# Optimization experiments

Measured on AMD Instinct MI355X. Metric: run time of the kernel, lower is better.

The kernel has to match this reference:

```python
import jax, jax.numpy as jnp
import numpy as np


def _knn(coords, k):
    # coords: [N, 3]. Returns indices of the k nearest neighbors (self excluded): [N, k]
    sq = jnp.sum(coords * coords, axis=1)
    d2 = sq[:, None] + sq[None, :] - 2.0 * (coords @ coords.T)  # [N, N]
    n = coords.shape[0]
    d2 = jnp.where(jnp.eye(n, dtype=bool), jnp.inf, d2)  # loop=False: no self edges
    _, idx = jax.lax.top_k(-d2, k)
    return idx


def setup_inputs() -> dict:
    key = jax.random.key(0)
    ks = jax.random.split(key, 7)
    B, N, C = 8, 4096, 6
    feats = jax.random.normal(ks[0], (B, N, C), dtype=jnp.float32)
    # Glorot-ish scaled weights; PyG GCNConv lin has no bias, bias added post-aggregation.
    W1 = jax.random.normal(ks[1], (6, 64), dtype=jnp.float32) * (1.0 / np.sqrt(6))
    b1 = jnp.zeros((64,), dtype=jnp.float32)
    W2 = jax.random.normal(ks[2], (64, 128), dtype=jnp.float32) * (1.0 / np.sqrt(64))
    b2 = jnp.zeros((128,), dtype=jnp.float32)
    Wf = jax.random.normal(ks[3], (128, 128), dtype=jnp.float32) * (1.0 / np.sqrt(128))
    bf = jnp.zeros((128,), dtype=jnp.float32)
    return {"feats": feats, "W1": W1, "b1": b1, "W2": W2, "b2": b2,
            "Wf": Wf, "bf": bf, "k": 16}


def reference(feats, W1, b1, W2, b2, Wf, bf, k):
    # feats: [B, N, C]; coords = first 3 channels.
    coords = feats[..., :3]
    nbr = jax.vmap(lambda c: _knn(c, k))(coords)  # [B, N, k]
    inv_deg = 1.0 / (k + 1)  # every node has exactly k in-edges + self loop (uniform sym norm)
    x = feats
    for W, b in ((W1, b1), (W2, b2)):
        h = x @ W  # [B, N, H]
        nb = jax.vmap(lambda hb, ib: hb[ib])(h, nbr)  # gather neighbor feats: [B, N, k, H]
        x = jax.nn.relu((nb.sum(axis=2) + h) * inv_deg + b)  # GCN aggregate + bias + ReLU
    return x @ Wf + bf  # [B, N, out_dim]
```

## Files before the change

kernel.cpp:

```cpp
#include <hip/hip_runtime.h>
#include <cstdint>
#include <cstddef>

#define NPTS 4096
#define KNN  16
#define INV_DEG (1.0f / 17.0f)
#define CAP  48
#define TS   1024

typedef unsigned long long u64;
typedef unsigned int u32;
typedef float v2f __attribute__((ext_vector_type(2)));

__device__ __forceinline__ u32 mapmono(float f) {
  u32 u = __float_as_uint(f);
  return u ^ ((u32)((int)u >> 31) | 0x80000000u);
}
__device__ __forceinline__ float unmapmono(u32 m) {
  u32 u = (m & 0x80000000u) ? (m ^ 0x80000000u) : ~m;
  return __uint_as_float(u);
}

__global__ __launch_bounds__(512) void knn_kernel(const float* __restrict__ feats,
                                                  int* __restrict__ nbr) {
#pragma clang fp contract(off)
  __shared__ float sx[TS], sy[TS], sz[TS];
  __shared__ u64 sbuf[8][4][64];

  const int b = blockIdx.x >> 7;
  const int pbase = (blockIdx.x & 127) * 32;
  const float* fb = feats + (size_t)b * NPTS * 6;
  const int wave = threadIdx.x >> 6;
  const int lane = threadIdx.x & 63;

  int ip[4];
  float xi[4], yi[4], zi[4], sqi[4], tau[4];
  u64 slot[4];
  int cnt[4];
#pragma unroll
  for (int p = 0; p < 4; ++p) {
    ip[p] = pbase + wave * 4 + p;
    const float* fr = fb + (size_t)ip[p] * 6;
    xi[p] = fr[0]; yi[p] = fr[1]; zi[p] = fr[2];
    sqi[p] = __fadd_rn(__fadd_rn(__fmul_rn(xi[p], xi[p]), __fmul_rn(yi[p], yi[p])),
                       __fmul_rn(zi[p], zi[p]));
    tau[p] = __uint_as_float(0x7f800000u);
    slot[p] = ~0ull;
    cnt[p] = 0;
  }

  auto flush = [&](int p, bool fin) {
    u64* wb = &sbuf[wave][p][0];
    if (lane >= cnt[p] && lane < CAP) wb[lane] = ~0ull;
    if (lane < KNN) wb[CAP + lane] = slot[p];
    u64 myk = wb[lane];
    if ((u32)myk == (u32)ip[p]) {
      myk = ~0ull;
      wb[lane] = ~0ull;
    }
    int rank = 0;
#pragma unroll
    for (int m = 0; m < 64; m += 4) {
      u64 k0 = wb[m], k1 = wb[m + 1], k2 = wb[m + 2], k3 = wb[m + 3];
      rank += (int)(k0 < myk) + (int)(k1 < myk) + (int)(k2 < myk) + (int)(k3 < myk);
    }
    if (fin) {
      if (rank < KNN)
        nbr[((size_t)(b * NPTS) + ip[p]) * KNN + rank] = (int)(u32)myk;
    } else {
      if (rank < KNN) wb[rank] = myk;
      u64 s15 = wb[15];
      if (lane < KNN) slot[p] = wb[lane];
      tau[p] = unmapmono((u32)(s15 >> 32));
    }
    cnt[p] = 0;
  };

  for (int tb = 0; tb < NPTS; tb += TS) {
    __syncthreads();
    for (int t = threadIdx.x; t < TS; t += 512) {
      const float* fr = fb + (size_t)(tb + t) * 6;
      sx[t] = fr[0]; sy[t] = fr[1]; sz[t] = fr[2];
    }
    __syncthreads();

    for (int jb0 = 0; jb0 < TS; jb0 += 64) {
      const int tl = jb0 + lane;
      const int j = tb + tl;
      const float cx = sx[tl], cy = sy[tl], cz = sz[tl];
      const float sqj = __fadd_rn(__fadd_rn(__fmul_rn(cx, cx), __fmul_rn(cy, cy)),
                                  __fmul_rn(cz, cz));
      const v2f cx2 = {cx, cx}, cy2 = {cy, cy}, cz2 = {cz, cz}, sq2 = {sqj, sqj};
      float d2s[4];
#pragma unroll
      for (int pp = 0; pp < 2; ++pp) {
        v2f X = {xi[2 * pp], xi[2 * pp + 1]};
        v2f Y = {yi[2 * pp], yi[2 * pp + 1]};
        v2f Z = {zi[2 * pp], zi[2 * pp + 1]};
        v2f SQ = {sqi[2 * pp], sqi[2 * pp + 1]};
        v2f dot = X * cx2;
        dot = __builtin_elementwise_fma(Y, cy2, dot);
        dot = __builtin_elementwise_fma(Z, cz2, dot);
        v2f two = {2.0f, 2.0f};
        v2f d2 = (SQ + sq2) - two * dot;
        d2s[2 * pp] = d2.x;
        d2s[2 * pp + 1] = d2.y;
      }
#pragma unroll
      for (int p = 0; p < 4; ++p) {
        const bool pred = d2s[p] <= tau[p];
        const u64 bal = __ballot(pred);
        if (bal) {
          const int npass = __popcll(bal);
          if (cnt[p] + npass > CAP) flush(p, false);
          const int pos = cnt[p] + (int)__builtin_amdgcn_mbcnt_hi(
                                        (u32)(bal >> 32),
                                        __builtin_amdgcn_mbcnt_lo((u32)bal, 0));
          const u64 key = ((u64)mapmono(d2s[p]) << 32) | (u32)j;
          if (npass <= CAP) {
            if (pred) sbuf[wave][p][pos] = key;
            cnt[p] += npass;
          } else {
            if (pred && pos < CAP) sbuf[wave][p][pos] = key;
            cnt[p] = CAP;
            flush(p, false);
            if (pred && pos >= CAP) sbuf[wave][p][pos - CAP] = key;
            cnt[p] = npass - CAP;
          }
        }
      }
    }
  }
#pragma unroll
  for (int p = 0; p < 4; ++p) flush(p, true);
}

__global__ __launch_bounds__(256) void enc1_kernel(const float* __restrict__ feats,
                                                   const int* __restrict__ nbr,
                                                   const float* __restrict__ W1,
                                                   const float* __restrict__ b1,
                                                   float* __restrict__ x1) {
  __shared__ float af[64][6];
  const int tid = threadIdx.x;
  const int n0 = blockIdx.x * 64;
  const int gb = n0 & ~(NPTS - 1);

  if (tid < 128) {
    const int p = tid >> 1, h = tid & 1;
    const int n = n0 + p;
    const int d0 = h * 3;
    const int* nb = nbr + (size_t)n * KNN;
    const float* fr = feats + (size_t)n * 6 + d0;
    float a0 = fr[0], a1 = fr[1], a2 = fr[2];
#pragma unroll
    for (int t = 0; t < KNN; ++t) {
      const float* fq = feats + (size_t)(gb + nb[t]) * 6 + d0;
      a0 += fq[0]; a1 += fq[1]; a2 += fq[2];
    }
    af[p][d0] = a0; af[p][d0 + 1] = a1; af[p][d0 + 2] = a2;
  }
  __syncthreads();

  const int c = tid & 63, pg = tid >> 6;
  float w[6];
#pragma unroll
  for (int k = 0; k < 6; ++k) w[k] = W1[k * 64 + c];
  const float bv = b1[c];
  for (int pi = 0; pi < 16; ++pi) {
    const int p = pg * 16 + pi;
    float s = 0.f;
#pragma unroll
    for (int k = 0; k < 6; ++k) s = fmaf(af[p][k], w[k], s);
    x1[(size_t)(n0 + p) * 64 + c] = fmaxf(fmaf(s, INV_DEG, bv), 0.f);
  }
}

__global__ __launch_bounds__(256) void enc2_kernel(const float* __restrict__ x1,
                                                   const int* __restrict__ nbr,
                                                   const float* __restrict__ W2,
                                                   const float* __restrict__ b2,
                                                   float* __restrict__ x2) {
  __shared__ float a1s[16][64];
  __shared__ v2f w2s[64][64];
  const int tid = threadIdx.x;
  const int n0 = blockIdx.x * 16;
  const int gb = n0 & ~(NPTS - 1);

#pragma unroll
  for (int i = 0; i < 16; ++i) {
    const int e = tid + 256 * i;
    const int k = e >> 6, l = e & 63;
    v2f w;
    w.x = W2[k * 128 + l];
    w.y = W2[k * 128 + 64 + l];
    w2s[k][l] = w;
  }
  {
    const int p = tid >> 4, c4 = tid & 15;
    const int n = n0 + p;
    const int* nb = nbr + (size_t)n * KNN;
    float4 s = ((const float4*)(x1 + (size_t)n * 64))[c4];
#pragma unroll
    for (int t = 0; t < KNN; ++t) {
      float4 v = ((const float4*)(x1 + (size_t)(gb + nb[t]) * 64))[c4];
      s.x += v.x; s.y += v.y; s.z += v.z; s.w += v.w;
    }
    *((float4*)&a1s[p][c4 * 4]) = s;
  }
  __syncthreads();

  const int wave = tid >> 6, lane = tid & 63;
  const int p0 = wave * 4;
  const float bx = b2[lane], by = b2[lane + 64];
  v2f acc0 = {0, 0}, acc1 = {0, 0}, acc2 = {0, 0}, acc3 = {0, 0};
  for (int k = 0; k < 64; k += 4) {
    const float4 a0 = *(const float4*)&a1s[p0 + 0][k];
    const float4 a1v = *(const float4*)&a1s[p0 + 1][k];
    const float4 a2v = *(const float4*)&a1s[p0 + 2][k];
    const float4 a3v = *(const float4*)&a1s[p0 + 3][k];
#pragma unroll
    for (int kk = 0; kk < 4; ++kk) {
      const v2f w = w2s[k + kk][lane];
      const float e0 = kk == 0 ? a0.x : kk == 1 ? a0.y : kk == 2 ? a0.z : a0.w;
      const float e1 = kk == 0 ? a1v.x : kk == 1 ? a1v.y : kk == 2 ? a1v.z : a1v.w;
      const float e2 = kk == 0 ? a2v.x : kk == 1 ? a2v.y : kk == 2 ? a2v.z : a2v.w;
      const float e3 = kk == 0 ? a3v.x : kk == 1 ? a3v.y : kk == 2 ? a3v.z : a3v.w;
      v2f v0 = {e0, e0}, v1 = {e1, e1}, v2 = {e2, e2}, v3 = {e3, e3};
      acc0 = __builtin_elementwise_fma(v0, w, acc0);
      acc1 = __builtin_elementwise_fma(v1, w, acc1);
      acc2 = __builtin_elementwise_fma(v2, w, acc2);
      acc3 = __builtin_elementwise_fma(v3, w, acc3);
    }
  }
  v2f accs[4] = {acc0, acc1, acc2, acc3};
#pragma unroll
  for (int pi = 0; pi < 4; ++pi) {
    float* row = x2 + (size_t)(n0 + p0 + pi) * 128;
    row[lane] = fmaxf(fmaf(accs[pi].x, INV_DEG, bx), 0.f);
    row[lane + 64] = fmaxf(fmaf(accs[pi].y, INV_DEG, by), 0.f);
  }
}

__global__ __launch_bounds__(256) void enc3_kernel(const float* __restrict__ x2,
                                                   const float* __restrict__ Wf,
                                                   const float* __restrict__ bf,
                                                   float* __restrict__ out) {
  __shared__ float xs[16 * 128];
  __shared__ float part[2][16][128];
  const int tid = threadIdx.x;
  const int n0 = blockIdx.x * 16;

#pragma unroll
  for (int i = 0; i < 2; ++i) {
    const int e = tid + 256 * i;
    ((float4*)xs)[e] = ((const float4*)(x2 + (size_t)n0 * 128))[e];
  }

  const int wave = tid >> 6, lane = tid & 63;
  const int kh = wave & 1, pg = wave >> 1;
  v2f w[64];
#pragma unroll
  for (int j = 0; j < 64; ++j) {
    const int k = kh * 64 + j;
    w[j].x = Wf[k * 128 + lane];
    w[j].y = Wf[k * 128 + 64 + lane];
  }
  __syncthreads();

  for (int pi = 0; pi < 8; ++pi) {
    const int p = pg * 8 + pi;
    v2f acc = {0, 0};
    for (int j = 0; j < 64; j += 4) {
      const float4 a = *(const float4*)&xs[p * 128 + kh * 64 + j];
#pragma unroll
      for (int jj = 0; jj < 4; ++jj) {
        const float e = jj == 0 ? a.x : jj == 1 ? a.y : jj == 2 ? a.z : a.w;
        v2f v = {e, e};
        acc = __builtin_elementwise_fma(v, w[j + jj], acc);
      }
    }
    part[kh][p][lane] = acc.x;
    part[kh][p][lane + 64] = acc.y;
  }
  __syncthreads();

#pragma unroll
  for (int i = 0; i < 8; ++i) {
    const int e = tid + 256 * i;
    const int p = e >> 7, c = e & 127;
    out[(size_t)(n0 + p) * 128 + c] = part[0][p][c] + part[1][p][c] + bf[c];
  }
}

extern "C" void kernel_launch(void* const* d_in, const int* in_sizes, int n_in,
                              void* d_out, int out_size, void* d_ws, size_t ws_size,
                              hipStream_t stream) {
  const float* feats = (const float*)d_in[0];
  const float* W1 = (const float*)d_in[1];
  const float* b1 = (const float*)d_in[2];
  const float* W2 = (const float*)d_in[3];
  const float* b2 = (const float*)d_in[4];
  const float* Wf = (const float*)d_in[5];
  const float* bf = (const float*)d_in[6];
  float* out = (float*)d_out;

  char* ws = (char*)d_ws;
  int* nbr = (int*)ws;
  float* x1 = (float*)(ws + (size_t)(2 << 20));
  float* x2 = out;

  knn_kernel<<<1024, 512, 0, stream>>>(feats, nbr);
  enc1_kernel<<<512, 256, 0, stream>>>(feats, nbr, W1, b1, x1);
  enc2_kernel<<<2048, 256, 0, stream>>>(x1, nbr, W2, b2, x2);
  enc3_kernel<<<2048, 256, 0, stream>>>(x2, Wf, bf, out);
}
```

Baseline: 247.2 us.

## Halve KNN queries per wave and precompute candidate norms in LDS

```diff
diff --git a/kernel.cpp b/kernel.cpp
--- a/kernel.cpp
+++ b/kernel.cpp
@@ -6,7 +6,7 @@
 #define KNN  16
 #define INV_DEG (1.0f / 17.0f)
 #define CAP  48
-#define TS   1024
+#define TS   512
 
 typedef unsigned long long u64;
 typedef unsigned int u32;
@@ -24,22 +24,22 @@
 __global__ __launch_bounds__(512) void knn_kernel(const float* __restrict__ feats,
                                                   int* __restrict__ nbr) {
 #pragma clang fp contract(off)
-  __shared__ float sx[TS], sy[TS], sz[TS];
-  __shared__ u64 sbuf[8][4][64];
-
-  const int b = blockIdx.x >> 7;
-  const int pbase = (blockIdx.x & 127) * 32;
+  __shared__ float4 sc[TS];
+  __shared__ u64 sbuf[8][2][64];
+
+  const int b = blockIdx.x >> 8;
+  const int pbase = (blockIdx.x & 255) * 16;
   const float* fb = feats + (size_t)b * NPTS * 6;
   const int wave = threadIdx.x >> 6;
   const int lane = threadIdx.x & 63;
 
-  int ip[4];
-  float xi[4], yi[4], zi[4], sqi[4], tau[4];
-  u64 slot[4];
-  int cnt[4];
-#pragma unroll
-  for (int p = 0; p < 4; ++p) {
-    ip[p] = pbase + wave * 4 + p;
+  int ip[2];
+  float xi[2], yi[2], zi[2], sqi[2], tau[2];
+  u64 slot[2];
+  int cnt[2];
+#pragma unroll
+  for (int p = 0; p < 2; ++p) {
+    ip[p] = pbase + wave * 2 + p;
     const float* fr = fb + (size_t)ip[p] * 6;
     xi[p] = fr[0]; yi[p] = fr[1]; zi[p] = fr[2];
     sqi[p] = __fadd_rn(__fadd_rn(__fmul_rn(xi[p], xi[p]), __fmul_rn(yi[p], yi[p])),
@@ -80,34 +80,32 @@
     __syncthreads();
     for (int t = threadIdx.x; t < TS; t += 512) {
       const float* fr = fb + (size_t)(tb + t) * 6;
-      sx[t] = fr[0]; sy[t] = fr[1]; sz[t] = fr[2];
+      const float x = fr[0], y = fr[1], z = fr[2];
+      const float sq = __fadd_rn(__fadd_rn(__fmul_rn(x, x), __fmul_rn(y, y)),
+                                 __fmul_rn(z, z));
+      float4 c; c.x = x; c.y = y; c.z = z; c.w = sq;
+      sc[t] = c;
     }
     __syncthreads();
 
     for (int jb0 = 0; jb0 < TS; jb0 += 64) {
       const int tl = jb0 + lane;
       const int j = tb + tl;
-      const float cx = sx[tl], cy = sy[tl], cz = sz[tl];
-      const float sqj = __fadd_rn(__fadd_rn(__fmul_rn(cx, cx), __fmul_rn(cy, cy)),
-                                  __fmul_rn(cz, cz));
-      const v2f cx2 = {cx, cx}, cy2 = {cy, cy}, cz2 = {cz, cz}, sq2 = {sqj, sqj};
-      float d2s[4];
-#pragma unroll
-      for (int pp = 0; pp < 2; ++pp) {
-        v2f X = {xi[2 * pp], xi[2 * pp + 1]};
-        v2f Y = {yi[2 * pp], yi[2 * pp + 1]};
-        v2f Z = {zi[2 * pp], zi[2 * pp + 1]};
-        v2f SQ = {sqi[2 * pp], sqi[2 * pp + 1]};
-        v2f dot = X * cx2;
-        dot = __builtin_elementwise_fma(Y, cy2, dot);
-        dot = __builtin_elementwise_fma(Z, cz2, dot);
-        v2f two = {2.0f, 2.0f};
-        v2f d2 = (SQ + sq2) - two * dot;
-        d2s[2 * pp] = d2.x;
-        d2s[2 * pp + 1] = d2.y;
-      }
-#pragma unroll
-      for (int p = 0; p < 4; ++p) {
+      const float4 c = sc[tl];
+      const v2f cx2 = {c.x, c.x}, cy2 = {c.y, c.y}, cz2 = {c.z, c.z},
+                sq2 = {c.w, c.w};
+      v2f X = {xi[0], xi[1]};
+      v2f Y = {yi[0], yi[1]};
+      v2f Z = {zi[0], zi[1]};
+      v2f SQ = {sqi[0], sqi[1]};
+      v2f dot = X * cx2;
+      dot = __builtin_elementwise_fma(Y, cy2, dot);
+      dot = __builtin_elementwise_fma(Z, cz2, dot);
+      v2f two = {2.0f, 2.0f};
+      v2f d2v = (SQ + sq2) - two * dot;
+      float d2s[2] = {d2v.x, d2v.y};
+#pragma unroll
+      for (int p = 0; p < 2; ++p) {
         const bool pred = d2s[p] <= tau[p];
         const u64 bal = __ballot(pred);
         if (bal) {
@@ -132,7 +130,7 @@
     }
   }
 #pragma unroll
-  for (int p = 0; p < 4; ++p) flush(p, true);
+  for (int p = 0; p < 2; ++p) flush(p, true);
 }
 
 __global__ __launch_bounds__(256) void enc1_kernel(const float* __restrict__ feats,
@@ -309,7 +307,7 @@
   float* x1 = (float*)(ws + (size_t)(2 << 20));
   float* x2 = out;
 
-  knn_kernel<<<1024, 512, 0, stream>>>(feats, nbr);
+  knn_kernel<<<2048, 512, 0, stream>>>(feats, nbr);
   enc1_kernel<<<512, 256, 0, stream>>>(feats, nbr, W1, b1, x1);
   enc2_kernel<<<2048, 256, 0, stream>>>(x1, nbr, W2, b2, x2);
   enc3_kernel<<<2048, 256, 0, stream>>>(x2, Wf, bf, out);
```

Result: faster. 233.6 us (-5.5%).
